# Kernel tuning notes

Hardware: AMD Instinct MI355X
Metric: run time of the kernel (lower is better)

Reference implementation:

```python
import jax, jax.numpy as jnp
import numpy as np

EPS = 1e-12

def _l2norm(x):
    # F.normalize(x, dim=1): x / max(||x||_2, eps)
    n = jnp.sqrt(jnp.sum(x * x, axis=1, keepdims=True))
    return x / jnp.maximum(n, EPS)

def setup_inputs() -> dict:
    key = jax.random.key(0)
    ks = jax.random.split(key, 8)
    n_users, n_entities, channel = 100000, 100000, 128
    n_edges, n_inter, n_rel_rows = 600000, 500000, 15
    return {
        "user_emb": jax.random.normal(ks[0], (n_users, channel), dtype=jnp.float32),
        "item_emb": jax.random.normal(ks[1], (n_entities, channel), dtype=jnp.float32) * 0.1,
        "edge_index": jax.random.randint(ks[2], (2, n_edges), 0, n_entities, dtype=jnp.int64),
        "edge_type": jax.random.randint(ks[3], (n_edges,), 1, n_rel_rows + 1, dtype=jnp.int64),
        "inter_edge": jnp.stack([
            jax.random.randint(ks[4], (n_inter,), 0, n_users, dtype=jnp.int64),
            jax.random.randint(ks[5], (n_inter,), 0, n_entities, dtype=jnp.int64),
        ]),
        "inter_edge_w": jax.random.uniform(ks[6], (n_inter,), dtype=jnp.float32),
        "relation_emb": jax.random.normal(ks[7], (n_rel_rows, channel), dtype=jnp.float32) * 0.1,
        "n_hops": 2,
    }

def reference(user_emb, item_emb, edge_index, edge_type, inter_edge, inter_edge_w, relation_emb, n_hops):
    head, tail = edge_index[0], edge_index[1]
    n_entities = item_emb.shape[0]
    n_users = user_emb.shape[0]

    ent = item_emb
    for _ in range(n_hops):
        he = ent[head]                       # [E, d] gather
        te = ent[tail]                       # [E, d] gather
        re = relation_emb[edge_type - 1]     # [E, d] gather
        # scores = exp(sum(h*r*t)) then scatter_softmax over head segments
        scores = jnp.exp(jnp.sum(he * re * te, axis=1))  # [E]
        smax = jax.ops.segment_max(scores, head, num_segments=n_entities)
        e = jnp.exp(scores - smax[head])
        denom = jax.ops.segment_sum(e, head, num_segments=n_entities)
        attn = e / denom[head]
        ent = jax.ops.segment_sum(attn[:, None] * te, head, num_segments=n_entities)
        # dropout in eval mode (identity), then F.normalize
        ent = _l2norm(ent)

    u_idx, i_idx = inter_edge[0], inter_edge[1]
    item_agg = inter_edge_w[:, None] * ent[i_idx]  # [Ninter, d]
    user_agg = jax.ops.segment_sum(item_agg, u_idx, num_segments=n_users)
    return (_l2norm(user_agg), ent)
```

## Files before the change

### kernel.cpp

```cpp
#include <hip/hip_runtime.h>
#include <math.h>

#define D 128
#define EPS 1e-12f
#define SCAN_NB 128
#define SCAN_TPB 256

template <int CTRL>
__device__ __forceinline__ float rorAdd(float v) {
    int t = __builtin_amdgcn_update_dpp(0, __float_as_int(v), CTRL, 0xF, 0xF, true);
    return v + __int_as_float(t);
}
__device__ __forceinline__ float groupSum16(float v) {
    v = rorAdd<0x121>(v);
    v = rorAdd<0x122>(v);
    v = rorAdd<0x124>(v);
    v = rorAdd<0x128>(v);
    return v;
}

__device__ __forceinline__ void unpack8(uint4 q, float* f) {
    f[0] = __uint_as_float(q.x << 16); f[1] = __uint_as_float(q.x & 0xFFFF0000u);
    f[2] = __uint_as_float(q.y << 16); f[3] = __uint_as_float(q.y & 0xFFFF0000u);
    f[4] = __uint_as_float(q.z << 16); f[5] = __uint_as_float(q.z & 0xFFFF0000u);
    f[6] = __uint_as_float(q.w << 16); f[7] = __uint_as_float(q.w & 0xFFFF0000u);
}
__device__ __forceinline__ unsigned bfpack2(float lo, float hi) {
    unsigned ul = __float_as_uint(lo), uh = __float_as_uint(hi);
    ul = (ul + 0x7FFFu + ((ul >> 16) & 1u)) >> 16;
    uh = (uh + 0x7FFFu + ((uh >> 16) & 1u)) & 0xFFFF0000u;
    return ul | uh;
}
__device__ __forceinline__ uint4 pack8(const float* f) {
    uint4 q;
    q.x = bfpack2(f[0], f[1]); q.y = bfpack2(f[2], f[3]);
    q.z = bfpack2(f[4], f[5]); q.w = bfpack2(f[6], f[7]);
    return q;
}

__global__ void k_zero(int4* __restrict__ p, int n4) {
    int i = blockIdx.x * blockDim.x + threadIdx.x;
    if (i < n4) p[i] = make_int4(0, 0, 0, 0);
}

__global__ void k_count_rank(const int* __restrict__ head, const int* __restrict__ u_idx,
                             int* __restrict__ counts_all, int* __restrict__ rank,
                             int E, int Ninter, int N_ent) {
    int i = blockIdx.x * blockDim.x + threadIdx.x;
    if (i < E) rank[i] = atomicAdd(&counts_all[head[i]], 1);
    else if (i < E + Ninter) rank[i] = atomicAdd(&counts_all[N_ent + u_idx[i - E]], 1);
}

__global__ void k_count_both(const int* __restrict__ head, const int* __restrict__ u_idx,
                             int* __restrict__ counts_all, int E, int Ninter, int N_ent) {
    int i = blockIdx.x * blockDim.x + threadIdx.x;
    if (i < E) atomicAdd(&counts_all[head[i]], 1);
    else if (i < E + Ninter) atomicAdd(&counts_all[N_ent + u_idx[i - E]], 1);
}

__global__ void k_scan_block(const int* __restrict__ counts, int* __restrict__ bsum,
                             int N, int K) {
    __shared__ int lds[SCAN_TPB];
    int tid = threadIdx.x;
    int base = (blockIdx.x * SCAN_TPB + tid) * K;
    int s = 0;
    for (int k = 0; k < K; ++k) { int idx = base + k; if (idx < N) s += counts[idx]; }
    lds[tid] = s;
    __syncthreads();
    for (int off = SCAN_TPB / 2; off > 0; off >>= 1) {
        if (tid < off) lds[tid] += lds[tid + off];
        __syncthreads();
    }
    if (tid == 0) bsum[blockIdx.x] = lds[0];
}

__global__ void k_scan_top(int* __restrict__ bsum) {
    __shared__ int lds[SCAN_NB];
    int t = threadIdx.x;
    if (t < SCAN_NB) lds[t] = bsum[t];
    __syncthreads();
    if (t == 0) {
        int run = 0;
        for (int i = 0; i < SCAN_NB; ++i) { int c = lds[i]; lds[i] = run; run += c; }
    }
    __syncthreads();
    if (t < SCAN_NB) bsum[t] = lds[t];
}

__global__ void k_scan_final(const int* __restrict__ counts, const int* __restrict__ bsum,
                             int* __restrict__ row_start, int N, int K) {
    __shared__ int lds[SCAN_TPB];
    int tid = threadIdx.x;
    int base = (blockIdx.x * SCAN_TPB + tid) * K;
    int s = 0;
    for (int k = 0; k < K; ++k) { int idx = base + k; if (idx < N) s += counts[idx]; }
    lds[tid] = s;
    __syncthreads();
    for (int off = 1; off < SCAN_TPB; off <<= 1) {
        int v = (tid >= off) ? lds[tid - off] : 0;
        __syncthreads();
        lds[tid] += v;
        __syncthreads();
    }
    int run = lds[tid] - s + bsum[blockIdx.x];
    for (int k = 0; k < K; ++k) {
        int idx = base + k;
        if (idx <= N) {
            row_start[idx] = run;
            if (idx < N) run += counts[idx];
        }
    }
}

__global__ void k_reorder_rank(const int* __restrict__ head, const int* __restrict__ tail,
                               const int* __restrict__ etype,
                               const int* __restrict__ u_idx, const int* __restrict__ i_idx,
                               const float* __restrict__ w,
                               const int* __restrict__ rs_all, const int* __restrict__ rank,
                               int* __restrict__ packed, int2* __restrict__ riw,
                               int E, int Ninter, int N_ent) {
    int i = blockIdx.x * blockDim.x + threadIdx.x;
    if (i < E) {
        int h = head[i];
        packed[rs_all[h] + rank[i]] = tail[i] | ((etype[i] - 1) << 24);
    } else if (i < E + Ninter) {
        int k = i - E;
        int u = N_ent + u_idx[k];
        int pos = rs_all[u] + rank[i] - E;
        riw[pos] = make_int2(i_idx[k], __float_as_int(w[k]));
    }
}

__global__ void k_reorder_both(const int* __restrict__ head, const int* __restrict__ tail,
                               const int* __restrict__ etype,
                               const int* __restrict__ u_idx, const int* __restrict__ i_idx,
                               const float* __restrict__ w,
                               const int* __restrict__ rs_all, int* __restrict__ cursor,
                               int* __restrict__ packed, int2* __restrict__ riw,
                               int E, int Ninter, int N_ent) {
    int i = blockIdx.x * blockDim.x + threadIdx.x;
    if (i < E) {
        int h = head[i];
        int pos = rs_all[h] + atomicAdd(&cursor[h], 1);
        packed[pos] = tail[i] | ((etype[i] - 1) << 24);
    } else if (i < E + Ninter) {
        int k = i - E;
        int u = N_ent + u_idx[k];
        int pos = rs_all[u] + atomicAdd(&cursor[u], 1) - E;
        riw[pos] = make_int2(i_idx[k], __float_as_int(w[k]));
    }
}

__global__ void k_to_bf16(const float* __restrict__ in, uint4* __restrict__ out, int n8) {
    int i = blockIdx.x * blockDim.x + threadIdx.x;
    if (i >= n8) return;
    const float4* ip = (const float4*)in + (size_t)i * 2;
    float4 a = ip[0], b = ip[1];
    float f[8] = {a.x, a.y, a.z, a.w, b.x, b.y, b.z, b.w};
    out[i] = pack8(f);
}

__global__ void k_hop_bf16(const uint4* __restrict__ ent16,
                           const float* __restrict__ rel,
                           const int* __restrict__ rs_all,
                           const int* __restrict__ packed,
                           float* __restrict__ out_f32,
                           uint4* __restrict__ out_bf16,
                           int N) {
    int lane = threadIdx.x & 63;
    int l16 = lane & 15;
    int row = ((blockIdx.x * blockDim.x + threadIdx.x) >> 6) * 4 + (lane >> 4);
    if (row >= N) return;

    int rs = rs_all[row];
    int deg = rs_all[row + 1] - rs;

    float hv[8];
    unpack8(ent16[(size_t)row * 16 + l16], hv);

    float acc[8] = {0, 0, 0, 0, 0, 0, 0, 0};
    for (int j = 0; j < deg; ++j) {
        int p = packed[rs + j];
        uint4 t16 = ent16[(size_t)(p & 0xFFFFFF) * 16 + l16];
        const float4* rp = (const float4*)(rel + (size_t)(((unsigned)p) >> 24) * D);
        float4 ra = rp[l16 * 2], rb = rp[l16 * 2 + 1];
        float tv[8];
        unpack8(t16, tv);
        float v = hv[0] * ra.x * tv[0] + hv[1] * ra.y * tv[1] +
                  hv[2] * ra.z * tv[2] + hv[3] * ra.w * tv[3] +
                  hv[4] * rb.x * tv[4] + hv[5] * rb.y * tv[5] +
                  hv[6] * rb.z * tv[6] + hv[7] * rb.w * tv[7];
        v = groupSum16(v);
        float wgt = __expf(__expf(v));
#pragma unroll
        for (int k = 0; k < 8; ++k) acc[k] += wgt * tv[k];
    }

    float part = 0.f;
#pragma unroll
    for (int k = 0; k < 8; ++k) part += acc[k] * acc[k];
    float ss = groupSum16(part);
    float inv = 1.0f / fmaxf(sqrtf(ss), EPS);
#pragma unroll
    for (int k = 0; k < 8; ++k) acc[k] *= inv;

    if (out_f32) {
        float4* op = (float4*)(out_f32 + (size_t)row * D);
        op[l16 * 2]     = make_float4(acc[0], acc[1], acc[2], acc[3]);
        op[l16 * 2 + 1] = make_float4(acc[4], acc[5], acc[6], acc[7]);
    }
    if (out_bf16) out_bf16[(size_t)row * 16 + l16] = pack8(acc);
}

__global__ void k_user_bf16(const uint4* __restrict__ ent16,
                            const int* __restrict__ rs_all,
                            const int2* __restrict__ riw,
                            float* __restrict__ uout, int Nu, int N_ent, int E) {
    int lane = threadIdx.x & 63;
    int l16 = lane & 15;
    int row = ((blockIdx.x * blockDim.x + threadIdx.x) >> 6) * 4 + (lane >> 4);
    if (row >= Nu) return;

    int base = rs_all[N_ent + row];
    int deg = rs_all[N_ent + row + 1] - base;
    int rs = base - E;

    float acc[8] = {0, 0, 0, 0, 0, 0, 0, 0};
    for (int j = 0; j < deg; ++j) {
        int2 pw = riw[rs + j];
        float ww = __int_as_float(pw.y);
        uint4 t16 = ent16[(size_t)pw.x * 16 + l16];
        float tv[8];
        unpack8(t16, tv);
#pragma unroll
        for (int k = 0; k < 8; ++k) acc[k] += ww * tv[k];
    }
    float part = 0.f;
#pragma unroll
    for (int k = 0; k < 8; ++k) part += acc[k] * acc[k];
    float ss = groupSum16(part);
    float inv = 1.0f / fmaxf(sqrtf(ss), EPS);
#pragma unroll
    for (int k = 0; k < 8; ++k) acc[k] *= inv;
    float4* op = (float4*)(uout + (size_t)row * D);
    op[l16 * 2]     = make_float4(acc[0], acc[1], acc[2], acc[3]);
    op[l16 * 2 + 1] = make_float4(acc[4], acc[5], acc[6], acc[7]);
}

__global__ void k_hop_f32(const float* __restrict__ ent_in,
                          const float* __restrict__ rel,
                          const int* __restrict__ rs_all,
                          const int* __restrict__ packed,
                          float* __restrict__ ent_out, int N) {
    int lane = threadIdx.x & 63;
    int l16 = lane & 15;
    int row = ((blockIdx.x * blockDim.x + threadIdx.x) >> 6) * 4 + (lane >> 4);
    if (row >= N) return;
    int rs = rs_all[row];
    int deg = rs_all[row + 1] - rs;
    const float4* hp = (const float4*)(ent_in + (size_t)row * D);
    float4 ha = hp[l16], hb = hp[l16 + 16];
    float4 acca = make_float4(0, 0, 0, 0), accb = make_float4(0, 0, 0, 0);
    for (int j = 0; j < deg; ++j) {
        int p = packed[rs + j];
        const float4* tp = (const float4*)(ent_in + (size_t)(p & 0xFFFFFF) * D);
        const float4* rp = (const float4*)(rel + (size_t)(((unsigned)p) >> 24) * D);
        float4 ta = tp[l16], tb = tp[l16 + 16];
        float4 ra = rp[l16], rb = rp[l16 + 16];
        float v = ha.x * ra.x * ta.x + ha.y * ra.y * ta.y +
                  ha.z * ra.z * ta.z + ha.w * ra.w * ta.w +
                  hb.x * rb.x * tb.x + hb.y * rb.y * tb.y +
                  hb.z * rb.z * tb.z + hb.w * rb.w * tb.w;
        v = groupSum16(v);
        float wgt = __expf(__expf(v));
        acca.x += wgt * ta.x; acca.y += wgt * ta.y;
        acca.z += wgt * ta.z; acca.w += wgt * ta.w;
        accb.x += wgt * tb.x; accb.y += wgt * tb.y;
        accb.z += wgt * tb.z; accb.w += wgt * tb.w;
    }
    float part = acca.x * acca.x + acca.y * acca.y + acca.z * acca.z + acca.w * acca.w +
                 accb.x * accb.x + accb.y * accb.y + accb.z * accb.z + accb.w * accb.w;
    float ss = groupSum16(part);
    float inv = 1.0f / fmaxf(sqrtf(ss), EPS);
    acca.x *= inv; acca.y *= inv; acca.z *= inv; acca.w *= inv;
    accb.x *= inv; accb.y *= inv; accb.z *= inv; accb.w *= inv;
    float4* op = (float4*)(ent_out + (size_t)row * D);
    op[l16] = acca;
    op[l16 + 16] = accb;
}

__global__ void k_user_f32(const float* __restrict__ ent,
                           const int* __restrict__ rs_all,
                           const int2* __restrict__ riw,
                           float* __restrict__ uout, int Nu, int N_ent, int E) {
    int lane = threadIdx.x & 63;
    int l16 = lane & 15;
    int row = ((blockIdx.x * blockDim.x + threadIdx.x) >> 6) * 4 + (lane >> 4);
    if (row >= Nu) return;
    int base = rs_all[N_ent + row];
    int deg = rs_all[N_ent + row + 1] - base;
    int rs = base - E;
    float4 acca = make_float4(0, 0, 0, 0), accb = make_float4(0, 0, 0, 0);
    for (int j = 0; j < deg; ++j) {
        int2 pw = riw[rs + j];
        float ww = __int_as_float(pw.y);
        const float4* ip = (const float4*)(ent + (size_t)pw.x * D);
        float4 ta = ip[l16], tb = ip[l16 + 16];
        acca.x += ww * ta.x; acca.y += ww * ta.y;
        acca.z += ww * ta.z; acca.w += ww * ta.w;
        accb.x += ww * tb.x; accb.y += ww * tb.y;
        accb.z += ww * tb.z; accb.w += ww * tb.w;
    }
    float part = acca.x * acca.x + acca.y * acca.y + acca.z * acca.z + acca.w * acca.w +
                 accb.x * accb.x + accb.y * accb.y + accb.z * accb.z + accb.w * accb.w;
    float ss = groupSum16(part);
    float inv = 1.0f / fmaxf(sqrtf(ss), EPS);
    acca.x *= inv; acca.y *= inv; acca.z *= inv; acca.w *= inv;
    accb.x *= inv; accb.y *= inv; accb.z *= inv; accb.w *= inv;
    float4* op = (float4*)(uout + (size_t)row * D);
    op[l16] = acca;
    op[l16 + 16] = accb;
}

extern "C" void kernel_launch(void* const* d_in, const int* in_sizes, int n_in,
                              void* d_out, int out_size, void* d_ws, size_t ws_size,
                              hipStream_t stream) {
    const float* item_emb  = (const float*)d_in[1];
    const int*   edge_idx  = (const int*)d_in[2];
    const int*   edge_type = (const int*)d_in[3];
    const int*   inter     = (const int*)d_in[4];
    const float* inter_w   = (const float*)d_in[5];
    const float* rel       = (const float*)d_in[6];

    const int N_users = in_sizes[0] / D;
    const int N_ent   = in_sizes[1] / D;
    const int E       = in_sizes[2] / 2;
    const int Ninter  = in_sizes[5];
    const int N_tot   = N_ent + N_users;
    const int n_keys  = E + Ninter;

    float* user_out = (float*)d_out;
    float* ent_out  = (float*)d_out + (size_t)N_users * D;

    const int* head  = edge_idx;
    const int* tail  = edge_idx + E;
    const int* u_idx = inter;
    const int* i_idx = inter + Ninter;

    const int TPB = 256;
    dim3 blk(TPB);

    const size_t mir_u4 = (size_t)N_ent * 16;
    uint4* mirA     = (uint4*)d_ws;
    uint4* mirB     = mirA + mir_u4;
    int2* riw       = (int2*)(mirB + mir_u4);
    int* counts_all = (int*)(riw + Ninter);
    int* rs_all     = counts_all + N_tot;
    int* packed     = rs_all + N_tot + 1;
    int* bsum       = packed + E;
    int* rank       = bsum + SCAN_NB;

    size_t ints_b   = ((size_t)Ninter * 2 + N_tot * 2 + 1 + E + SCAN_NB + n_keys) * 4;
    size_t need_b16 = mir_u4 * 2 * 16 + ints_b;
    bool use_b16 = ws_size >= need_b16;

    if (!use_b16) {
        riw        = (int2*)d_ws;
        counts_all = (int*)(riw + Ninter);
        rs_all     = counts_all + N_tot;
        packed     = rs_all + N_tot + 1;
        bsum       = packed + E;
        rank       = bsum + SCAN_NB;
    }
    bool use_rank = use_b16 || ws_size >= ints_b;

    int K = (N_tot + SCAN_NB * SCAN_TPB - 1) / (SCAN_NB * SCAN_TPB);

    int n4 = N_tot / 4;
    k_zero<<<(n4 + TPB - 1) / TPB, blk, 0, stream>>>((int4*)counts_all, n4);

    if (use_rank) {
        k_count_rank<<<(n_keys + TPB - 1) / TPB, blk, 0, stream>>>(
            head, u_idx, counts_all, rank, E, Ninter, N_ent);
        k_scan_block<<<SCAN_NB, SCAN_TPB, 0, stream>>>(counts_all, bsum, N_tot, K);
        k_scan_top<<<1, SCAN_TPB, 0, stream>>>(bsum);
        k_scan_final<<<SCAN_NB, SCAN_TPB, 0, stream>>>(counts_all, bsum, rs_all, N_tot, K);
        k_reorder_rank<<<(n_keys + TPB - 1) / TPB, blk, 0, stream>>>(
            head, tail, edge_type, u_idx, i_idx, inter_w,
            rs_all, rank, packed, riw, E, Ninter, N_ent);
    } else {
        k_count_both<<<(n_keys + TPB - 1) / TPB, blk, 0, stream>>>(
            head, u_idx, counts_all, E, Ninter, N_ent);
        k_scan_block<<<SCAN_NB, SCAN_TPB, 0, stream>>>(counts_all, bsum, N_tot, K);
        k_scan_top<<<1, SCAN_TPB, 0, stream>>>(bsum);
        k_scan_final<<<SCAN_NB, SCAN_TPB, 0, stream>>>(counts_all, bsum, rs_all, N_tot, K);
        k_zero<<<(n4 + TPB - 1) / TPB, blk, 0, stream>>>((int4*)counts_all, n4);
        k_reorder_both<<<(n_keys + TPB - 1) / TPB, blk, 0, stream>>>(
            head, tail, edge_type, u_idx, i_idx, inter_w,
            rs_all, counts_all, packed, riw, E, Ninter, N_ent);
    }

    int grid_rows  = (N_ent + 15) / 16;
    int grid_users = (N_users + 15) / 16;

    if (use_b16) {
        int n8 = N_ent * (D / 8);
        k_to_bf16<<<(n8 + TPB - 1) / TPB, blk, 0, stream>>>(item_emb, mirA, n8);
        k_hop_bf16<<<grid_rows, blk, 0, stream>>>(
            mirA, rel, rs_all, packed, nullptr, mirB, N_ent);
        k_hop_bf16<<<grid_rows, blk, 0, stream>>>(
            mirB, rel, rs_all, packed, ent_out, mirA, N_ent);
        k_user_bf16<<<grid_users, blk, 0, stream>>>(
            mirA, rs_all, riw, user_out, N_users, N_ent, E);
    } else {
        float* ent_mid = user_out;
        k_hop_f32<<<grid_rows, blk, 0, stream>>>(item_emb, rel, rs_all, packed, ent_mid, N_ent);
        k_hop_f32<<<grid_rows, blk, 0, stream>>>(ent_mid, rel, rs_all, packed, ent_out, N_ent);
        k_user_f32<<<grid_users, blk, 0, stream>>>(
            ent_out, rs_all, riw, user_out, N_users, N_ent, E);
    }
}
```

Baseline: 209.6 us.

## Fuse bf16 conversion into count kernel and software-prefetch neighbor gathers

The fp32-to-bf16 conversion of item embeddings now runs inside the counting/rank kernel as extra threads, which removes one launch and lets the streaming conversion overlap the atomic counting. The hop and user aggregation loops now prefetch the next neighbor's index, embedding row and relation row before computing on the current one, so gather latency overlaps the arithmetic. The cost is more live registers, which may lower occupancy.

```diff
diff --git a/kernel.cpp b/kernel.cpp
--- a/kernel.cpp
+++ b/kernel.cpp
@@ -43,12 +43,23 @@
     if (i < n4) p[i] = make_int4(0, 0, 0, 0);
 }
 
-__global__ void k_count_rank(const int* __restrict__ head, const int* __restrict__ u_idx,
+__global__ void k_count_conv(const int* __restrict__ head, const int* __restrict__ u_idx,
                              int* __restrict__ counts_all, int* __restrict__ rank,
-                             int E, int Ninter, int N_ent) {
-    int i = blockIdx.x * blockDim.x + threadIdx.x;
-    if (i < E) rank[i] = atomicAdd(&counts_all[head[i]], 1);
-    else if (i < E + Ninter) rank[i] = atomicAdd(&counts_all[N_ent + u_idx[i - E]], 1);
+                             const float* __restrict__ emb, uint4* __restrict__ mir,
+                             int E, int Ninter, int N_ent, int n8) {
+    int i = blockIdx.x * blockDim.x + threadIdx.x;
+    int n_keys = E + Ninter;
+    if (i < E) {
+        rank[i] = atomicAdd(&counts_all[head[i]], 1);
+    } else if (i < n_keys) {
+        rank[i] = atomicAdd(&counts_all[N_ent + u_idx[i - E]], 1);
+    } else if (i < n_keys + n8) {
+        int c = i - n_keys;
+        const float4* ip = (const float4*)emb + (size_t)c * 2;
+        float4 a = ip[0], b = ip[1];
+        float f[8] = {a.x, a.y, a.z, a.w, b.x, b.y, b.z, b.w};
+        mir[c] = pack8(f);
+    }
 }
 
 __global__ void k_count_both(const int* __restrict__ head, const int* __restrict__ u_idx,
@@ -179,21 +190,31 @@
     unpack8(ent16[(size_t)row * 16 + l16], hv);
 
     float acc[8] = {0, 0, 0, 0, 0, 0, 0, 0};
-    for (int j = 0; j < deg; ++j) {
-        int p = packed[rs + j];
+    if (deg > 0) {
+        int p = packed[rs];
         uint4 t16 = ent16[(size_t)(p & 0xFFFFFF) * 16 + l16];
         const float4* rp = (const float4*)(rel + (size_t)(((unsigned)p) >> 24) * D);
         float4 ra = rp[l16 * 2], rb = rp[l16 * 2 + 1];
-        float tv[8];
-        unpack8(t16, tv);
-        float v = hv[0] * ra.x * tv[0] + hv[1] * ra.y * tv[1] +
-                  hv[2] * ra.z * tv[2] + hv[3] * ra.w * tv[3] +
-                  hv[4] * rb.x * tv[4] + hv[5] * rb.y * tv[5] +
-                  hv[6] * rb.z * tv[6] + hv[7] * rb.w * tv[7];
-        v = groupSum16(v);
-        float wgt = __expf(__expf(v));
-#pragma unroll
-        for (int k = 0; k < 8; ++k) acc[k] += wgt * tv[k];
+        for (int j = 0; j < deg; ++j) {
+            uint4 ct16 = t16;
+            float4 cra = ra, crb = rb;
+            if (j + 1 < deg) {
+                int pn = packed[rs + j + 1];
+                t16 = ent16[(size_t)(pn & 0xFFFFFF) * 16 + l16];
+                rp = (const float4*)(rel + (size_t)(((unsigned)pn) >> 24) * D);
+                ra = rp[l16 * 2]; rb = rp[l16 * 2 + 1];
+            }
+            float tv[8];
+            unpack8(ct16, tv);
+            float v = hv[0] * cra.x * tv[0] + hv[1] * cra.y * tv[1] +
+                      hv[2] * cra.z * tv[2] + hv[3] * cra.w * tv[3] +
+                      hv[4] * crb.x * tv[4] + hv[5] * crb.y * tv[5] +
+                      hv[6] * crb.z * tv[6] + hv[7] * crb.w * tv[7];
+            v = groupSum16(v);
+            float wgt = __expf(__expf(v));
+#pragma unroll
+            for (int k = 0; k < 8; ++k) acc[k] += wgt * tv[k];
+        }
     }
 
     float part = 0.f;
@@ -226,14 +247,23 @@
     int rs = base - E;
 
     float acc[8] = {0, 0, 0, 0, 0, 0, 0, 0};
-    for (int j = 0; j < deg; ++j) {
-        int2 pw = riw[rs + j];
+    if (deg > 0) {
+        int2 pw = riw[rs];
+        uint4 t16 = ent16[(size_t)pw.x * 16 + l16];
         float ww = __int_as_float(pw.y);
-        uint4 t16 = ent16[(size_t)pw.x * 16 + l16];
-        float tv[8];
-        unpack8(t16, tv);
-#pragma unroll
-        for (int k = 0; k < 8; ++k) acc[k] += ww * tv[k];
+        for (int j = 0; j < deg; ++j) {
+            uint4 ct16 = t16;
+            float cw = ww;
+            if (j + 1 < deg) {
+                int2 pn = riw[rs + j + 1];
+                t16 = ent16[(size_t)pn.x * 16 + l16];
+                ww = __int_as_float(pn.y);
+            }
+            float tv[8];
+            unpack8(ct16, tv);
+#pragma unroll
+            for (int k = 0; k < 8; ++k) acc[k] += cw * tv[k];
+        }
     }
     float part = 0.f;
 #pragma unroll
@@ -375,37 +405,23 @@
     bool use_rank = use_b16 || ws_size >= ints_b;
 
     int K = (N_tot + SCAN_NB * SCAN_TPB - 1) / (SCAN_NB * SCAN_TPB);
-
     int n4 = N_tot / 4;
+    int n8 = N_ent * (D / 8);
+
     k_zero<<<(n4 + TPB - 1) / TPB, blk, 0, stream>>>((int4*)counts_all, n4);
 
-    if (use_rank) {
-        k_count_rank<<<(n_keys + TPB - 1) / TPB, blk, 0, stream>>>(
-            head, u_idx, counts_all, rank, E, Ninter, N_ent);
+    if (use_b16) {
+        k_count_conv<<<(n_keys + n8 + TPB - 1) / TPB, blk, 0, stream>>>(
+            head, u_idx, counts_all, rank, item_emb, mirA, E, Ninter, N_ent, n8);
         k_scan_block<<<SCAN_NB, SCAN_TPB, 0, stream>>>(counts_all, bsum, N_tot, K);
         k_scan_top<<<1, SCAN_TPB, 0, stream>>>(bsum);
         k_scan_final<<<SCAN_NB, SCAN_TPB, 0, stream>>>(counts_all, bsum, rs_all, N_tot, K);
         k_reorder_rank<<<(n_keys + TPB - 1) / TPB, blk, 0, stream>>>(
             head, tail, edge_type, u_idx, i_idx, inter_w,
             rs_all, rank, packed, riw, E, Ninter, N_ent);
-    } else {
-        k_count_both<<<(n_keys + TPB - 1) / TPB, blk, 0, stream>>>(
-            head, u_idx, counts_all, E, Ninter, N_ent);
-        k_scan_block<<<SCAN_NB, SCAN_TPB, 0, stream>>>(counts_all, bsum, N_tot, K);
-        k_scan_top<<<1, SCAN_TPB, 0, stream>>>(bsum);
-        k_scan_final<<<SCAN_NB, SCAN_TPB, 0, stream>>>(counts_all, bsum, rs_all, N_tot, K);
-        k_zero<<<(n4 + TPB - 1) / TPB, blk, 0, stream>>>((int4*)counts_all, n4);
-        k_reorder_both<<<(n_keys + TPB - 1) / TPB, blk, 0, stream>>>(
-            head, tail, edge_type, u_idx, i_idx, inter_w,
-            rs_all, counts_all, packed, riw, E, Ninter, N_ent);
-    }
-
-    int grid_rows  = (N_ent + 15) / 16;
-    int grid_users = (N_users + 15) / 16;
-
-    if (use_b16) {
-        int n8 = N_ent * (D / 8);
-        k_to_bf16<<<(n8 + TPB - 1) / TPB, blk, 0, stream>>>(item_emb, mirA, n8);
+
+        int grid_rows  = (N_ent + 15) / 16;
+        int grid_users = (N_users + 15) / 16;
         k_hop_bf16<<<grid_rows, blk, 0, stream>>>(
             mirA, rel, rs_all, packed, nullptr, mirB, N_ent);
         k_hop_bf16<<<grid_rows, blk, 0, stream>>>(
@@ -413,6 +429,28 @@
         k_user_bf16<<<grid_users, blk, 0, stream>>>(
             mirA, rs_all, riw, user_out, N_users, N_ent, E);
     } else {
+        if (use_rank) {
+            k_count_conv<<<(n_keys + TPB - 1) / TPB, blk, 0, stream>>>(
+                head, u_idx, counts_all, rank, nullptr, nullptr, E, Ninter, N_ent, 0);
+            k_scan_block<<<SCAN_NB, SCAN_TPB, 0, stream>>>(counts_all, bsum, N_tot, K);
+            k_scan_top<<<1, SCAN_TPB, 0, stream>>>(bsum);
+            k_scan_final<<<SCAN_NB, SCAN_TPB, 0, stream>>>(counts_all, bsum, rs_all, N_tot, K);
+            k_reorder_rank<<<(n_keys + TPB - 1) / TPB, blk, 0, stream>>>(
+                head, tail, edge_type, u_idx, i_idx, inter_w,
+                rs_all, rank, packed, riw, E, Ninter, N_ent);
+        } else {
+            k_count_both<<<(n_keys + TPB - 1) / TPB, blk, 0, stream>>>(
+                head, u_idx, counts_all, E, Ninter, N_ent);
+            k_scan_block<<<SCAN_NB, SCAN_TPB, 0, stream>>>(counts_all, bsum, N_tot, K);
+            k_scan_top<<<1, SCAN_TPB, 0, stream>>>(bsum);
+            k_scan_final<<<SCAN_NB, SCAN_TPB, 0, stream>>>(counts_all, bsum, rs_all, N_tot, K);
+            k_zero<<<(n4 + TPB - 1) / TPB, blk, 0, stream>>>((int4*)counts_all, n4);
+            k_reorder_both<<<(n_keys + TPB - 1) / TPB, blk, 0, stream>>>(
+                head, tail, edge_type, u_idx, i_idx, inter_w,
+                rs_all, counts_all, packed, riw, E, Ninter, N_ent);
+        }
+        int grid_rows  = (N_ent + 15) / 16;
+        int grid_users = (N_users + 15) / 16;
         float* ent_mid = user_out;
         k_hop_f32<<<grid_rows, blk, 0, stream>>>(item_emb, rel, rs_all, packed, ent_mid, N_ent);
         k_hop_f32<<<grid_rows, blk, 0, stream>>>(ent_mid, rel, rs_all, packed, ent_out, N_ent);
```

Result: faster. 205.4 us (-2.0%).
